# Performance work log

Measured on AMD Instinct MI355X. Metric: run time of the kernel, lower is better.

The kernel has to match this reference:

```python
import jax, jax.numpy as jnp
import numpy as np

# Perfect 8-ary tree, 6 levels, level-order node indexing.
K = 8            # children per internal node
D = 512          # embedding_dim
P = 8            # number of dependency types (num_params)
OFF = [0, 1, 9, 73, 585, 4681, 37449]  # level start offsets; N = 37449
N = OFF[-1]


def setup_inputs() -> dict:
    key = jax.random.key(0)
    ks = jax.random.split(key, 8)
    s = 1.0 / np.sqrt(D)  # torch default-ish init scale, avoids LSTM saturation
    return {
        "embeddings": jax.random.normal(ks[0], (N, D), dtype=jnp.float32),
        "dep_types": jax.random.randint(ks[1], (N,), 0, P, dtype=jnp.int32),
        "W_dep": jax.random.normal(ks[2], (P, D, D), dtype=jnp.float32) * s,
        "b_dep": jax.random.normal(ks[3], (P, D), dtype=jnp.float32) * s,
        "W_ih": jax.random.normal(ks[4], (4 * D, D), dtype=jnp.float32) * s,
        "W_hh": jax.random.normal(ks[5], (4 * D, D), dtype=jnp.float32) * s,
        "b_ih": jax.random.normal(ks[6], (4 * D,), dtype=jnp.float32) * s,
        "b_hh": jax.random.normal(ks[7], (4 * D,), dtype=jnp.float32) * s,
    }


def _lstm_final_c(seq, W_ih, W_hh, b_ih, b_hh):
    # seq: [B, T, D]; 1-layer LSTM with zero init state; returns final cell state c_T [B, D]
    B = seq.shape[0]
    h0 = jnp.zeros((B, D), seq.dtype)

    def step(carry, z_t):
        h, c = carry
        gates = z_t @ W_ih.T + h @ W_hh.T + b_ih + b_hh  # [B, 4D]
        i, f, g, o = jnp.split(gates, 4, axis=-1)        # torch gate order i,f,g,o
        i, f, o = jax.nn.sigmoid(i), jax.nn.sigmoid(f), jax.nn.sigmoid(o)
        g = jnp.tanh(g)
        c = f * c + i * g
        h = o * jnp.tanh(c)
        return (h, c), None

    (h, c), _ = jax.lax.scan(step, (h0, h0), jnp.swapaxes(seq, 0, 1))
    return c


def reference(embeddings, dep_types, W_dep, b_dep, W_ih, W_hh, b_ih, b_hh):
    # Leaves (level 5): LSTM over length-1 sequence [x] -> final cell state.
    leaf_x = embeddings[OFF[5]:OFF[6]]                       # [32768, D]
    z = _lstm_final_c(leaf_x[:, None, :], W_ih, W_hh, b_ih, b_hh)

    # Level-synchronous bottom-up sweep (exactly the recursion's per-node math).
    for l in range(4, -1, -1):
        m = OFF[l + 1] - OFF[l]                              # nodes at this level
        child_z = z.reshape(m, K, D)                         # children's subtree codes
        child_dep = dep_types[OFF[l + 1]:OFF[l + 2]].reshape(m, K)
        onehot = jax.nn.one_hot(child_dep, P, dtype=child_z.dtype)  # [m, K, P]
        # per-dep Linear: z_c = W_dep[dep] @ x_c + b_dep[dep]
        zc = jnp.einsum('mkj,pij,mkp->mki', child_z, W_dep, onehot) + onehot @ b_dep
        x = embeddings[OFF[l]:OFF[l + 1]]                    # node's own embedding, last in seq
        seq = jnp.concatenate([zc, x[:, None, :]], axis=1)   # [m, K+1, D]
        z = _lstm_final_c(seq, W_ih, W_hh, b_ih, b_hh)

    return z  # root sentence embedding, [1, D]
```

## Files before the change

kernel.cpp:

```cpp
#include <hip/hip_runtime.h>

typedef __attribute__((ext_vector_type(8))) short short8;
typedef __attribute__((ext_vector_type(4))) float f32x4;
typedef _Float16 half_t;

__device__ __forceinline__ unsigned short f2bf(float x){
  union { float f; unsigned u; } v; v.f = x;
  unsigned r = v.u + 0x7fffu + ((v.u >> 16) & 1u);
  return (unsigned short)(r >> 16);
}
__device__ __forceinline__ float sigm(float x){ return 1.0f / (1.0f + __expf(-x)); }
__device__ __forceinline__ float tanh_(float x){
  float e = __expf(2.0f * x);
  return 1.0f - 2.0f / (e + 1.0f);
}
__device__ __forceinline__ short8 load_bf8_f32(const float* p){
  float4 a = *(const float4*)p;
  float4 b = *(const float4*)(p + 4);
  short8 r;
  r[0]=(short)f2bf(a.x); r[1]=(short)f2bf(a.y); r[2]=(short)f2bf(a.z); r[3]=(short)f2bf(a.w);
  r[4]=(short)f2bf(b.x); r[5]=(short)f2bf(b.y); r[6]=(short)f2bf(b.z); r[7]=(short)f2bf(b.w);
  return r;
}
__device__ __forceinline__ f32x4 mfma16(short8 a, short8 b, f32x4 c){
  return __builtin_amdgcn_mfma_f32_16x16x32_bf16(a, b, c, 0, 0, 0);
}
__device__ __forceinline__ void gload16(const void* g, void* lds){
  __builtin_amdgcn_global_load_lds((const __attribute__((address_space(1))) void*)g,
                                   (__attribute__((address_space(3))) void*)lds, 16, 0, 0);
}
__device__ __forceinline__ f32x4 shfl_xor4(f32x4 v, int m){
  f32x4 r;
  r[0]=__shfl_xor(v[0],m); r[1]=__shfl_xor(v[1],m);
  r[2]=__shfl_xor(v[2],m); r[3]=__shfl_xor(v[3],m);
  return r;
}
__device__ __forceinline__ float pick4(f32x4 v, int k){
  float a = (k&1)? v[1] : v[0];
  float b = (k&1)? v[3] : v[2];
  return (k&2)? b : a;
}
__device__ __forceinline__ f32x4 sel4(f32x4 a0, f32x4 a1, f32x4 a2, f32x4 a3, int k){
  f32x4 x = (k&1)? a1 : a0;
  f32x4 y = (k&1)? a3 : a2;
  return (k&2)? y : x;
}

#define KLOOP_BODY(ABASE, BBASE)                                                     \
  for (int kt = 0; kt < 8; ++kt){                                                    \
    _Pragma("unroll")                                                                \
    for (int q = 0; q < 4; ++q){                                                     \
      gload16(ABASE[q] + kt*64, &As[(q*32 + w*8)*64]);                               \
      gload16(BBASE[q] + kt*64, &Bs[(q*32 + w*8)*64]);                               \
    }                                                                                \
    __syncthreads();                                                                 \
    _Pragma("unroll")                                                                \
    for (int kk = 0; kk < 2; ++kk){                                                  \
      short8 av[4], bv[4];                                                           \
      _Pragma("unroll")                                                              \
      for (int i = 0; i < 4; ++i) av[i] = *(const short8*)&As[(wm*64 + i*16 + r15)*64 + kk*32 + g4*8]; \
      _Pragma("unroll")                                                              \
      for (int i = 0; i < 4; ++i) bv[i] = *(const short8*)&Bs[(wn*64 + i*16 + r15)*64 + kk*32 + g4*8]; \
      _Pragma("unroll")                                                              \
      for (int i = 0; i < 4; ++i)                                                    \
        _Pragma("unroll")                                                            \
        for (int j = 0; j < 4; ++j) acc[i][j] = mfma16(av[i], bv[j], acc[i][j]);     \
    }                                                                                \
    __syncthreads();                                                                 \
  }

__global__ __launch_bounds__(256) void prep_kernel(
    const float* __restrict__ emb, const int* __restrict__ dep,
    const float* __restrict__ W_dep, const float* __restrict__ b_dep,
    const float* __restrict__ W_ih, const float* __restrict__ W_hh,
    const float* __restrict__ b_ih, const float* __restrict__ b_hh,
    unsigned short* __restrict__ embb, unsigned short* __restrict__ Wih_il,
    unsigned short* __restrict__ Whh_il, unsigned short* __restrict__ Wleaf,
    unsigned short* __restrict__ WdT, float* __restrict__ bsum, float* __restrict__ bc,
    int* __restrict__ perm, int* __restrict__ tile_p, int* __restrict__ meta)
{
  const int bid = blockIdx.x, tid = threadIdx.x;
  if (bid < 1024){
    for (size_t i = (size_t)bid*256 + tid; i < 2396736ull; i += 1024ull*256)
      *(short8*)(embb + i*8) = load_bf8_f32(emb + i*8);
  } else if (bid < 1536){
    int idx = (bid-1024)*256 + tid; int r = idx >> 6, c8 = idx & 63;
    int sr = (r & 3)*512 + (r >> 2);
    *(short8*)(Wih_il + (size_t)r*512 + c8*8) = load_bf8_f32(W_ih + (size_t)sr*512 + c8*8);
  } else if (bid < 2048){
    int idx = (bid-1536)*256 + tid; int r = idx >> 6, c8 = idx & 63;
    int sr = (r & 3)*512 + (r >> 2);
    *(short8*)(Whh_il + (size_t)r*512 + c8*8) = load_bf8_f32(W_hh + (size_t)sr*512 + c8*8);
  } else if (bid < 2304){
    int idx = (bid-2048)*256 + tid; int r = idx >> 6, c8 = idx & 63;
    int sr = ((r & 1) ? 2 : 0)*512 + (r >> 1);
    *(short8*)(Wleaf + (size_t)r*512 + c8*8) = load_bf8_f32(W_ih + (size_t)sr*512 + c8*8);
  } else if (bid < 2816){
    __shared__ unsigned short tle[64][65];
    int lb = bid - 2304; int p = lb >> 6; int tile = lb & 63;
    int i0 = (tile >> 3)*64, j0 = (tile & 7)*64;
    const float* src = W_dep + (size_t)p*512*512;
    for (int q = 0; q < 16; ++q){
      int e = q*256 + tid; int li = e >> 6, lj = e & 63;
      tle[li][lj] = f2bf(src[(size_t)(i0+li)*512 + (j0+lj)]);
    }
    __syncthreads();
    unsigned short* dst = WdT + (size_t)p*512*512;
    for (int q = 0; q < 16; ++q){
      int e = q*256 + tid; int lj = e >> 6, li = e & 63;
      dst[(size_t)(j0+lj)*512 + (i0+li)] = tle[li][lj];
    }
  } else if (bid < 2824){
    int r = (bid-2816)*256 + tid;
    if (r < 2048){ int g = r & 3, j = r >> 2; bsum[r] = b_ih[g*512+j] + b_hh[g*512+j]; }
  } else if (bid < 2888){
    __shared__ float bd[512];
    int lb = bid - 2824; int p = lb >> 3, ch = lb & 7;
    for (int i = tid; i < 512; i += 256) bd[i] = b_dep[p*512 + i];
    __syncthreads();
    int r = ch*256 + tid; int g = r & 3, j = r >> 2;
    const float* wr = W_ih + (size_t)(g*512 + j)*512;
    float s = 0.0f;
    for (int i = 0; i < 512; ++i) s = fmaf(wr[i], bd[i], s);
    bc[(size_t)p*2048 + r] = s;
  } else {
    __shared__ int cnt[8], base[8], fill[8];
    int lb = bid - 2888; const int l = lb >> 3, t = lb & 7;
    const int M_[5]  = {1,8,64,512,4096};
    const int CB_[5] = {1,9,73,585,4681};
    const int MT_[5] = {8,8,8,12,40};
    const int PB_[5] = {69632,61440,53248,40960,0};
    const int TB_[5] = {544,480,416,320,0};
    const int m = M_[l], cb = CB_[l], MT = MT_[l];
    int* pm = perm + PB_[l] + t*MT*128;
    int* tp = tile_p + TB_[l] + t*MT;
    if (tid < 8){ cnt[tid] = 0; fill[tid] = 0; }
    __syncthreads();
    for (int n = tid; n < m; n += 256) atomicAdd(&cnt[dep[cb + n*8 + t]], 1);
    __syncthreads();
    if (tid == 0){
      int tiles = 0;
      for (int p = 0; p < 8; ++p){
        base[p] = tiles*128;
        int g = (cnt[p] + 127) >> 7;
        for (int q = 0; q < g; ++q) tp[tiles + q] = p;
        tiles += g;
      }
      meta[l*8 + t] = tiles;
    }
    __syncthreads();
    for (int i = tid; i < MT*128; i += 256) pm[i] = -1;
    __syncthreads();
    for (int n = tid; n < m; n += 256){
      int p = dep[cb + n*8 + t];
      pm[base[p] + atomicAdd(&fill[p], 1)] = n;
    }
  }
}

__global__ __launch_bounds__(256) void combo_gemm(
    const unsigned short* __restrict__ A,
    const unsigned short* __restrict__ WdT,
    unsigned short* __restrict__ C)
{
  const int p  = blockIdx.x >> 6;
  const int mt = (blockIdx.x >> 2) & 15;
  const int nb = blockIdx.x & 3;
  __shared__ unsigned short As[128*64];
  __shared__ unsigned short Bs[128*64];
  const int tid = threadIdx.x, lane = tid & 63, w = tid >> 6;
  const int wm = w >> 1, wn = w & 1;
  const int r15 = lane & 15, g4 = lane >> 4;
  const int kc = (lane & 7)*8;

  const unsigned short* ab[4]; const unsigned short* bb[4];
  #pragma unroll
  for (int q = 0; q < 4; ++q){
    int rl = mt*128 + q*32 + w*8 + (lane >> 3);
    ab[q] = A + (size_t)rl*512 + kc;
    int br = nb*128 + q*32 + w*8 + (lane >> 3);
    bb[q] = WdT + (size_t)p*262144 + (size_t)br*512 + kc;
  }
  f32x4 acc[4][4] = {};
  KLOOP_BODY(ab, bb)
  unsigned short* Cp = C + (size_t)p*1048576;
  #pragma unroll
  for (int mi = 0; mi < 4; ++mi)
    #pragma unroll
    for (int ni = 0; ni < 4; ++ni)
      #pragma unroll
      for (int j = 0; j < 4; ++j){
        int row = mt*128 + wm*64 + mi*16 + g4*4 + j;
        int col = nb*128 + wn*64 + ni*16 + r15;
        Cp[(size_t)row*512 + col] = f2bf(acc[mi][ni][j]);
      }
}

__global__ __launch_bounds__(256) void leaf_gemm(
    const unsigned short* __restrict__ embL,
    const unsigned short* __restrict__ Wleaf,
    const float* __restrict__ bsum,
    unsigned short* __restrict__ zo)
{
  const int nb = blockIdx.x & 7;
  const int mt = blockIdx.x >> 3;
  __shared__ unsigned short As[128*64];
  __shared__ unsigned short Bs[128*64];
  const int tid = threadIdx.x, lane = tid & 63, w = tid >> 6;
  const int wm = w >> 1, wn = w & 1;
  const int r15 = lane & 15, g4 = lane >> 4;
  const int kc = (lane & 7)*8;

  const unsigned short* ab[4]; const unsigned short* bb[4];
  #pragma unroll
  for (int q = 0; q < 4; ++q){
    int rl = mt*128 + q*32 + w*8 + (lane >> 3);
    ab[q] = embL + (size_t)rl*512 + kc;
    int br = nb*128 + q*32 + w*8 + (lane >> 3);
    bb[q] = Wleaf + (size_t)br*512 + kc;
  }
  f32x4 acc[4][4] = {};
  KLOOP_BODY(ab, bb)
  const int g2 = r15 & 1;
  #pragma unroll
  for (int ni = 0; ni < 4; ++ni){
    int ci = nb*128 + wn*64 + ni*16 + r15;
    float b = bsum[4*(ci >> 1) + (g2 ? 2 : 0)];
    #pragma unroll
    for (int mi = 0; mi < 4; ++mi){
      acc[mi][ni][0]+=b; acc[mi][ni][1]+=b; acc[mi][ni][2]+=b; acc[mi][ni][3]+=b;
    }
  }
  #pragma unroll
  for (int mi = 0; mi < 4; ++mi)
    #pragma unroll
    for (int ni = 0; ni < 4; ++ni){
      f32x4 a0 = acc[mi][ni];
      f32x4 a1 = shfl_xor4(a0, 1);
      f32x4 vi_ = g2 ? a1 : a0;
      f32x4 vg_ = g2 ? a0 : a1;
      int jz = (nb*128 + wn*64 + ni*16 + r15) >> 1;
      #pragma unroll
      for (int u = 0; u < 2; ++u){
        int jrow = (g2 << 1) + u;
        float zi = pick4(vi_, jrow), zg = pick4(vg_, jrow);
        int row = mt*128 + wm*64 + mi*16 + g4*4 + jrow;
        zo[(size_t)row*512 + jz] = f2bf(sigm(zi) * tanh_(zg));
      }
    }
}

__device__ __forceinline__ void step_core(
    unsigned short* As, unsigned short* Bs,
    const unsigned short* __restrict__ embb,
    const unsigned short* __restrict__ Wcombo,
    const unsigned short* __restrict__ Wih_il,
    const unsigned short* __restrict__ Whh_il,
    const float* __restrict__ bsum, const float* __restrict__ bc,
    const unsigned short* __restrict__ zin, unsigned short* __restrict__ zo,
    const unsigned short* __restrict__ hi, unsigned short* __restrict__ ho,
    float* __restrict__ cbuf, float* __restrict__ outp,
    const int* __restrict__ pm, const int* __restrict__ tp,
    int node_base, int m, int t, int mt, int nbq, int l)
{
  const int tid = threadIdx.x, lane = tid & 63, w = tid >> 6;
  const int wm = w >> 1, wn = w & 1;
  const int r15 = lane & 15, g4 = lane >> 4;
  const int kc = (lane & 7)*8;
  const int first = (t == 0), last = (t == 8);
  const int p = tp ? tp[mt] : 0;

  int nn[4];
  #pragma unroll
  for (int q = 0; q < 4; ++q){
    int rl = mt*128 + q*32 + w*8 + (lane >> 3);
    int n = pm ? pm[rl] : (rl < m ? rl : -1);
    nn[q] = (n < 0) ? 0 : n;
  }
  f32x4 acc[4][4] = {};
  {
    const unsigned short* Bx = (t < 8) ? (Wcombo + (size_t)p*1048576) : Wih_il;
    const unsigned short* ab[4]; const unsigned short* bb[4];
    #pragma unroll
    for (int q = 0; q < 4; ++q){
      ab[q] = (t < 8) ? (zin + ((size_t)nn[q]*8 + t)*512 + kc)
                      : (embb + (size_t)(node_base + nn[q])*512 + kc);
      int br = nbq*128 + q*32 + w*8 + (lane >> 3);
      bb[q] = Bx + (size_t)br*512 + kc;
    }
    KLOOP_BODY(ab, bb)
  }
  if (!first){
    const unsigned short* ab[4]; const unsigned short* bb[4];
    #pragma unroll
    for (int q = 0; q < 4; ++q){
      ab[q] = hi + (size_t)nn[q]*512 + kc;
      int br = nbq*128 + q*32 + w*8 + (lane >> 3);
      bb[q] = Whh_il + (size_t)br*512 + kc;
    }
    KLOOP_BODY(ab, bb)
  }
  const int gate = r15 & 3;
  #pragma unroll
  for (int ni = 0; ni < 4; ++ni){
    int ci = nbq*128 + wn*64 + ni*16 + r15;
    float b = bsum[ci] + ((t < 8) ? bc[(size_t)p*2048 + ci] : 0.0f);
    #pragma unroll
    for (int mi = 0; mi < 4; ++mi){
      acc[mi][ni][0]+=b; acc[mi][ni][1]+=b; acc[mi][ni][2]+=b; acc[mi][ni][3]+=b;
    }
  }
  const int jr = r15 & 3;
  #pragma unroll
  for (int mi = 0; mi < 4; ++mi){
    int rl = mt*128 + wm*64 + mi*16 + g4*4 + jr;
    int n = pm ? pm[rl] : (rl < m ? rl : -1);
    #pragma unroll
    for (int ni = 0; ni < 4; ++ni){
      f32x4 a0 = acc[mi][ni];
      f32x4 a1 = shfl_xor4(a0, 1);
      f32x4 a2 = shfl_xor4(a0, 2);
      f32x4 a3 = shfl_xor4(a1, 2);
      f32x4 vi_ = sel4(a0,a1,a2,a3, gate);
      f32x4 vf_ = sel4(a0,a1,a2,a3, gate^1);
      f32x4 vg_ = sel4(a0,a1,a2,a3, gate^2);
      f32x4 vo_ = sel4(a0,a1,a2,a3, gate^3);
      float xi = pick4(vi_, jr), xf = pick4(vf_, jr);
      float xg = pick4(vg_, jr), xo = pick4(vo_, jr);
      if (n >= 0){
        int jz = nbq*32 + wn*16 + ni*4 + (r15 >> 2);
        size_t idx = (size_t)n*512 + jz;
        float i_ = sigm(xi), f_ = sigm(xf), g_ = tanh_(xg), o_ = sigm(xo);
        float cold = first ? 0.0f : cbuf[idx];
        float cn = fmaf(f_, cold, i_*g_);
        if (!last){ cbuf[idx] = cn; ho[idx] = f2bf(o_*tanh_(cn)); }
        else { if (l > 0) zo[idx] = f2bf(cn); else outp[idx] = cn; }
      }
    }
  }
}

__global__ __launch_bounds__(256) void step_kernel(
    const unsigned short* __restrict__ embb,
    const unsigned short* __restrict__ Wcombo,
    const unsigned short* __restrict__ Wih_il,
    const unsigned short* __restrict__ Whh_il,
    const float* __restrict__ bsum, const float* __restrict__ bc,
    const unsigned short* __restrict__ zin, unsigned short* __restrict__ zo,
    const unsigned short* __restrict__ hi, unsigned short* __restrict__ ho,
    float* __restrict__ cbuf, float* __restrict__ outp,
    const int* __restrict__ perm_t, const int* __restrict__ tile_t,
    const int* __restrict__ meta_t,
    int fixed_nt, int MTcap, int node_base, int m, int t, int l)
{
  __shared__ unsigned short As[128*64];
  __shared__ unsigned short Bs[128*64];
  int ntiles = meta_t ? *meta_t : fixed_nt;
  if (ntiles > MTcap) ntiles = MTcap;
  const int njobs = ntiles * 16;
  const int chunk = (njobs + 7) >> 3;
  const int g = blockIdx.x & 7, i = blockIdx.x >> 3;
  const int job = g*chunk + i;
  if (i >= chunk || job >= njobs) return;
  const int mt = job % ntiles, nbq = job / ntiles;
  step_core(As, Bs, embb, Wcombo, Wih_il, Whh_il, bsum, bc, zin, zo, hi, ho,
            cbuf, outp, perm_t, tile_t, node_base, m, t, mt, nbq, l);
}

__global__ __launch_bounds__(256) void gatex_kernel(
    const unsigned short* __restrict__ embb,
    const unsigned short* __restrict__ Wcombo,
    const unsigned short* __restrict__ Wih_il,
    const float* __restrict__ bsum, const float* __restrict__ bc,
    const unsigned short* __restrict__ zin,
    half_t* __restrict__ gx, unsigned short* __restrict__ h0out,
    float* __restrict__ cbuf,
    const int* __restrict__ perm_l, const int* __restrict__ tile_l,
    const int* __restrict__ meta_l,
    int MT, int m, int node_base)
{
  __shared__ unsigned short As[128*64];
  __shared__ unsigned short Bs[128*64];
  const int jt = blockIdx.x >> 4, nbq = blockIdx.x & 15;
  int t, mt, p = 0;
  const int* pm = nullptr;
  if (jt < 8*MT){
    t = jt / MT; mt = jt - t*MT;
    if (mt >= meta_l[t]) return;
    pm = perm_l + t*MT*128;
    p = tile_l[t*MT + mt];
  } else {
    t = 8; mt = jt - 8*MT;
  }
  const int tid = threadIdx.x, lane = tid & 63, w = tid >> 6;
  const int wm = w >> 1, wn = w & 1;
  const int r15 = lane & 15, g4 = lane >> 4;
  const int kc = (lane & 7)*8;

  int nn[4];
  #pragma unroll
  for (int q = 0; q < 4; ++q){
    int rl = mt*128 + q*32 + w*8 + (lane >> 3);
    int n = pm ? pm[rl] : (rl < m ? rl : -1);
    nn[q] = (n < 0) ? 0 : n;
  }
  const unsigned short* Bx = (t < 8) ? (Wcombo + (size_t)p*1048576) : Wih_il;
  const unsigned short* ab[4]; const unsigned short* bb[4];
  #pragma unroll
  for (int q = 0; q < 4; ++q){
    ab[q] = (t < 8) ? (zin + ((size_t)nn[q]*8 + t)*512 + kc)
                    : (embb + (size_t)(node_base + nn[q])*512 + kc);
    int br = nbq*128 + q*32 + w*8 + (lane >> 3);
    bb[q] = Bx + (size_t)br*512 + kc;
  }
  f32x4 acc[4][4] = {};
  KLOOP_BODY(ab, bb)

  #pragma unroll
  for (int ni = 0; ni < 4; ++ni){
    int ci = nbq*128 + wn*64 + ni*16 + r15;
    float b = bsum[ci] + ((t < 8) ? bc[(size_t)p*2048 + ci] : 0.0f);
    #pragma unroll
    for (int mi = 0; mi < 4; ++mi){
      acc[mi][ni][0]+=b; acc[mi][ni][1]+=b; acc[mi][ni][2]+=b; acc[mi][ni][3]+=b;
    }
  }

  if (t == 0){
    const int gate = r15 & 3;
    const int jr = r15 & 3;
    #pragma unroll
    for (int mi = 0; mi < 4; ++mi){
      int rl = mt*128 + wm*64 + mi*16 + g4*4 + jr;
      int n = pm ? pm[rl] : (rl < m ? rl : -1);
      #pragma unroll
      for (int ni = 0; ni < 4; ++ni){
        f32x4 a0 = acc[mi][ni];
        f32x4 a1 = shfl_xor4(a0, 1);
        f32x4 a2 = shfl_xor4(a0, 2);
        f32x4 a3 = shfl_xor4(a1, 2);
        f32x4 vi_ = sel4(a0,a1,a2,a3, gate);
        f32x4 vg_ = sel4(a0,a1,a2,a3, gate^2);
        f32x4 vo_ = sel4(a0,a1,a2,a3, gate^3);
        float xi = pick4(vi_, jr);
        float xg = pick4(vg_, jr);
        float xo = pick4(vo_, jr);
        if (n >= 0){
          int jz = nbq*32 + wn*16 + ni*4 + (r15 >> 2);
          size_t idx = (size_t)n*512 + jz;
          float cn = sigm(xi) * tanh_(xg);
          cbuf[idx] = cn;
          h0out[idx] = f2bf(sigm(xo) * tanh_(cn));
        }
      }
    }
  } else {
    #pragma unroll
    for (int mi = 0; mi < 4; ++mi)
      #pragma unroll
      for (int ni = 0; ni < 4; ++ni){
        int ci = nbq*128 + wn*64 + ni*16 + r15;
        #pragma unroll
        for (int j = 0; j < 4; ++j){
          int rl = mt*128 + wm*64 + mi*16 + g4*4 + j;
          int n = pm ? pm[rl] : (rl < m ? rl : -1);
          if (n >= 0) gx[((size_t)t*m + n)*2048 + ci] = (half_t)acc[mi][ni][j];
        }
      }
  }
}

__global__ __launch_bounds__(256) void hstep_kernel(
    const unsigned short* __restrict__ Whh_il,
    const half_t* __restrict__ gx,
    const unsigned short* __restrict__ hi, unsigned short* __restrict__ ho,
    float* __restrict__ cbuf,
    unsigned short* __restrict__ zo, float* __restrict__ outp,
    int m, int t, int last)
{
  __shared__ unsigned short As[128*64];
  __shared__ unsigned short Bs[128*64];
  const int mt = blockIdx.x >> 4, nbq = blockIdx.x & 15;
  const int tid = threadIdx.x, lane = tid & 63, w = tid >> 6;
  const int wm = w >> 1, wn = w & 1;
  const int r15 = lane & 15, g4 = lane >> 4;
  const int kc = (lane & 7)*8;

  int nn[4];
  #pragma unroll
  for (int q = 0; q < 4; ++q){
    int rl = mt*128 + q*32 + w*8 + (lane >> 3);
    nn[q] = (rl < m) ? rl : 0;
  }
  const unsigned short* ab[4]; const unsigned short* bb[4];
  #pragma unroll
  for (int q = 0; q < 4; ++q){
    ab[q] = hi + (size_t)nn[q]*512 + kc;
    int br = nbq*128 + q*32 + w*8 + (lane >> 3);
    bb[q] = Whh_il + (size_t)br*512 + kc;
  }
  f32x4 acc[4][4] = {};
  KLOOP_BODY(ab, bb)

  #pragma unroll
  for (int mi = 0; mi < 4; ++mi)
    #pragma unroll
    for (int ni = 0; ni < 4; ++ni){
      int ci = nbq*128 + wn*64 + ni*16 + r15;
      #pragma unroll
      for (int j = 0; j < 4; ++j){
        int rl = mt*128 + wm*64 + mi*16 + g4*4 + j;
        if (rl < m) acc[mi][ni][j] += (float)gx[((size_t)t*m + rl)*2048 + ci];
      }
    }

  const int gate = r15 & 3;
  const int jr = r15 & 3;
  #pragma unroll
  for (int mi = 0; mi < 4; ++mi){
    int rl = mt*128 + wm*64 + mi*16 + g4*4 + jr;
    int n = (rl < m) ? rl : -1;
    #pragma unroll
    for (int ni = 0; ni < 4; ++ni){
      f32x4 a0 = acc[mi][ni];
      f32x4 a1 = shfl_xor4(a0, 1);
      f32x4 a2 = shfl_xor4(a0, 2);
      f32x4 a3 = shfl_xor4(a1, 2);
      f32x4 vi_ = sel4(a0,a1,a2,a3, gate);
      f32x4 vf_ = sel4(a0,a1,a2,a3, gate^1);
      f32x4 vg_ = sel4(a0,a1,a2,a3, gate^2);
      f32x4 vo_ = sel4(a0,a1,a2,a3, gate^3);
      float xi = pick4(vi_, jr), xf = pick4(vf_, jr);
      float xg = pick4(vg_, jr), xo = pick4(vo_, jr);
      if (n >= 0){
        int jz = nbq*32 + wn*16 + ni*4 + (r15 >> 2);
        size_t idx = (size_t)n*512 + jz;
        float i_ = sigm(xi), f_ = sigm(xf), g_ = tanh_(xg), o_ = sigm(xo);
        float cn = fmaf(f_, cbuf[idx], i_*g_);
        if (!last){ cbuf[idx] = cn; ho[idx] = f2bf(o_*tanh_(cn)); }
        else { if (zo) zo[idx] = f2bf(cn); else outp[idx] = cn; }
      }
    }
  }
}

extern "C" void kernel_launch(void* const* d_in, const int* in_sizes, int n_in,
                              void* d_out, int out_size, void* d_ws, size_t ws_size,
                              hipStream_t stream)
{
  (void)in_sizes; (void)n_in; (void)out_size; (void)ws_size;
  const float* emb   = (const float*)d_in[0];
  const int*   dep   = (const int*)  d_in[1];
  const float* W_dep = (const float*)d_in[2];
  const float* b_dep = (const float*)d_in[3];
  const float* W_ih  = (const float*)d_in[4];
  const float* W_hh  = (const float*)d_in[5];
  const float* b_ih  = (const float*)d_in[6];
  const float* b_hh  = (const float*)d_in[7];
  float* out = (float*)d_out;

  unsigned short* embb   = (unsigned short*)d_ws;
  unsigned short* Wih_il = embb   + 19173888ull;
  unsigned short* Whh_il = Wih_il + 1048576ull;
  unsigned short* Wleaf  = Whh_il + 1048576ull;
  unsigned short* WdT    = Wleaf  + 524288ull;
  unsigned short* Wcombo = WdT    + 2097152ull;
  unsigned short* Z0     = Wcombo + 8388608ull;
  unsigned short* Z1     = Z0     + 16777216ull;
  unsigned short* hA     = Z1     + 2097152ull;
  unsigned short* hB     = hA     + 2097152ull;
  float* cbuf  = (float*)(hB + 2097152ull);
  float* bsum  = cbuf + 2097152ull;
  float* bc    = bsum + 2048;
  int*  perm   = (int*)(bc + 16384);
  int*  tile_p = perm + 77824;
  int*  meta   = tile_p + 608;
  half_t* gx   = (half_t*)(meta + 40);

  prep_kernel<<<2928, 256, 0, stream>>>(emb, dep, W_dep, b_dep, W_ih, W_hh, b_ih, b_hh,
                                        embb, Wih_il, Whh_il, Wleaf, WdT, bsum, bc,
                                        perm, tile_p, meta);
  combo_gemm<<<512, 256, 0, stream>>>(Wih_il, WdT, Wcombo);
  leaf_gemm<<<2048, 256, 0, stream>>>(embb + (size_t)4681*512, Wleaf, bsum, Z0);

  for (int t = 0; t <= 8; ++t){
    const unsigned short* hi = (t & 1) ? hA : hB;
    unsigned short* ho       = (t & 1) ? hB : hA;
    int grid = (t < 8) ? 40*16 : 32*16;
    step_kernel<<<grid, 256, 0, stream>>>(
        embb, Wcombo, Wih_il, Whh_il, bsum, bc,
        Z0, Z1, hi, ho, cbuf, nullptr,
        (t < 8) ? (perm + t*40*128) : nullptr,
        (t < 8) ? (tile_p + t*40) : nullptr,
        (t < 8) ? (meta + 4*8 + t) : nullptr,
        32, 40, 585, 4096, t, 4);
  }

  struct LvP { int m, MT, PB, TB, nb_, mtiles; };
  const LvP LP[4] = {
    {512, 12, 40960, 320, 73, 4},
    {64,  8,  53248, 416, 9,  1},
    {8,   8,  61440, 480, 1,  1},
    {1,   8,  69632, 544, 0,  1}};
  for (int k = 0; k < 4; ++k){
    const int l = 3 - k;
    const unsigned short* zin = (l & 1) ? Z1 : Z0;
    unsigned short* zo        = (l & 1) ? Z0 : Z1;
    gatex_kernel<<<(8*LP[k].MT + LP[k].mtiles)*16, 256, 0, stream>>>(
        embb, Wcombo, Wih_il, bsum, bc, zin, gx, hA, cbuf,
        perm + LP[k].PB, tile_p + LP[k].TB, meta + l*8,
        LP[k].MT, LP[k].m, LP[k].nb_);
    for (int t = 1; t <= 8; ++t){
      const unsigned short* hi = (t & 1) ? hA : hB;
      unsigned short* ho       = (t & 1) ? hB : hA;
      hstep_kernel<<<LP[k].mtiles*16, 256, 0, stream>>>(
          Whh_il, gx, hi, ho, cbuf,
          (l > 0) ? zo : nullptr, (l == 0) ? out : nullptr,
          LP[k].m, t, (t == 8));
    }
  }
}
```

Baseline: 1.539 ms.

## Double-buffer LDS tiles and XOR-swizzle layout in shared GEMM k-loop

The shared k-loop macro now keeps two LDS buffers per operand and issues the global-to-LDS loads for the next k-tile before computing on the current one. This overlaps memory latency with MFMA work and drops one barrier per iteration. The global load column offset is also XOR-swizzled by row, with matching swizzled LDS reads, to cut bank conflicts. LDS per block doubles to 64 KB, which may lower occupancy.

```diff
diff --git a/kernel.cpp b/kernel.cpp
--- a/kernel.cpp
+++ b/kernel.cpp
@@ -47,26 +47,41 @@
 }
 
 #define KLOOP_BODY(ABASE, BBASE)                                                     \
-  for (int kt = 0; kt < 8; ++kt){                                                    \
+  {                                                                                  \
     _Pragma("unroll")                                                                \
     for (int q = 0; q < 4; ++q){                                                     \
-      gload16(ABASE[q] + kt*64, &As[(q*32 + w*8)*64]);                               \
-      gload16(BBASE[q] + kt*64, &Bs[(q*32 + w*8)*64]);                               \
+      gload16(ABASE[q], As + (q*32 + w*8)*64);                                       \
+      gload16(BBASE[q], Bs + (q*32 + w*8)*64);                                       \
     }                                                                                \
     __syncthreads();                                                                 \
-    _Pragma("unroll")                                                                \
-    for (int kk = 0; kk < 2; ++kk){                                                  \
-      short8 av[4], bv[4];                                                           \
+    for (int kt = 0; kt < 8; ++kt){                                                  \
+      unsigned short* Ac = As + (kt & 1)*8192;                                       \
+      unsigned short* Bc = Bs + (kt & 1)*8192;                                       \
+      if (kt < 7){                                                                   \
+        unsigned short* An = As + ((kt + 1) & 1)*8192;                               \
+        unsigned short* Bn = Bs + ((kt + 1) & 1)*8192;                               \
+        _Pragma("unroll")                                                            \
+        for (int q = 0; q < 4; ++q){                                                 \
+          gload16(ABASE[q] + (kt+1)*64, An + (q*32 + w*8)*64);                       \
+          gload16(BBASE[q] + (kt+1)*64, Bn + (q*32 + w*8)*64);                       \
+        }                                                                            \
+      }                                                                              \
       _Pragma("unroll")                                                              \
-      for (int i = 0; i < 4; ++i) av[i] = *(const short8*)&As[(wm*64 + i*16 + r15)*64 + kk*32 + g4*8]; \
-      _Pragma("unroll")                                                              \
-      for (int i = 0; i < 4; ++i) bv[i] = *(const short8*)&Bs[(wn*64 + i*16 + r15)*64 + kk*32 + g4*8]; \
-      _Pragma("unroll")                                                              \
-      for (int i = 0; i < 4; ++i)                                                    \
+      for (int kk = 0; kk < 2; ++kk){                                                \
+        short8 av[4], bv[4];                                                         \
         _Pragma("unroll")                                                            \
-        for (int j = 0; j < 4; ++j) acc[i][j] = mfma16(av[i], bv[j], acc[i][j]);     \
+        for (int i = 0; i < 4; ++i)                                                  \
+          av[i] = *(const short8*)&Ac[(wm*64 + i*16 + r15)*64 + (((kk*4 + g4) ^ (r15 & 7))*8)]; \
+        _Pragma("unroll")                                                            \
+        for (int i = 0; i < 4; ++i)                                                  \
+          bv[i] = *(const short8*)&Bc[(wn*64 + i*16 + r15)*64 + (((kk*4 + g4) ^ (r15 & 7))*8)]; \
+        _Pragma("unroll")                                                            \
+        for (int i = 0; i < 4; ++i)                                                  \
+          _Pragma("unroll")                                                          \
+          for (int j = 0; j < 4; ++j) acc[i][j] = mfma16(av[i], bv[j], acc[i][j]);   \
+      }                                                                              \
+      __syncthreads();                                                               \
     }                                                                                \
-    __syncthreads();                                                                 \
   }
 
 __global__ __launch_bounds__(256) void prep_kernel(
@@ -166,12 +181,12 @@
   const int p  = blockIdx.x >> 6;
   const int mt = (blockIdx.x >> 2) & 15;
   const int nb = blockIdx.x & 3;
-  __shared__ unsigned short As[128*64];
-  __shared__ unsigned short Bs[128*64];
+  __shared__ unsigned short As[16384];
+  __shared__ unsigned short Bs[16384];
   const int tid = threadIdx.x, lane = tid & 63, w = tid >> 6;
   const int wm = w >> 1, wn = w & 1;
   const int r15 = lane & 15, g4 = lane >> 4;
-  const int kc = (lane & 7)*8;
+  const int kc = ((lane & 7) ^ (lane >> 3)) * 8;
 
   const unsigned short* ab[4]; const unsigned short* bb[4];
   #pragma unroll
@@ -204,12 +219,12 @@
 {
   const int nb = blockIdx.x & 7;
   const int mt = blockIdx.x >> 3;
-  __shared__ unsigned short As[128*64];
-  __shared__ unsigned short Bs[128*64];
+  __shared__ unsigned short As[16384];
+  __shared__ unsigned short Bs[16384];
   const int tid = threadIdx.x, lane = tid & 63, w = tid >> 6;
   const int wm = w >> 1, wn = w & 1;
   const int r15 = lane & 15, g4 = lane >> 4;
-  const int kc = (lane & 7)*8;
+  const int kc = ((lane & 7) ^ (lane >> 3)) * 8;
 
   const unsigned short* ab[4]; const unsigned short* bb[4];
   #pragma unroll
@@ -266,7 +281,7 @@
   const int tid = threadIdx.x, lane = tid & 63, w = tid >> 6;
   const int wm = w >> 1, wn = w & 1;
   const int r15 = lane & 15, g4 = lane >> 4;
-  const int kc = (lane & 7)*8;
+  const int kc = ((lane & 7) ^ (lane >> 3)) * 8;
   const int first = (t == 0), last = (t == 8);
   const int p = tp ? tp[mt] : 0;
 
@@ -353,8 +368,8 @@
     const int* __restrict__ meta_t,
     int fixed_nt, int MTcap, int node_base, int m, int t, int l)
 {
-  __shared__ unsigned short As[128*64];
-  __shared__ unsigned short Bs[128*64];
+  __shared__ unsigned short As[16384];
+  __shared__ unsigned short Bs[16384];
   int ntiles = meta_t ? *meta_t : fixed_nt;
   if (ntiles > MTcap) ntiles = MTcap;
   const int njobs = ntiles * 16;
@@ -379,8 +394,8 @@
     const int* __restrict__ meta_l,
     int MT, int m, int node_base)
 {
-  __shared__ unsigned short As[128*64];
-  __shared__ unsigned short Bs[128*64];
+  __shared__ unsigned short As[16384];
+  __shared__ unsigned short Bs[16384];
   const int jt = blockIdx.x >> 4, nbq = blockIdx.x & 15;
   int t, mt, p = 0;
   const int* pm = nullptr;
@@ -395,7 +410,7 @@
   const int tid = threadIdx.x, lane = tid & 63, w = tid >> 6;
   const int wm = w >> 1, wn = w & 1;
   const int r15 = lane & 15, g4 = lane >> 4;
-  const int kc = (lane & 7)*8;
+  const int kc = ((lane & 7) ^ (lane >> 3)) * 8;
 
   int nn[4];
   #pragma unroll
@@ -478,13 +493,13 @@
     unsigned short* __restrict__ zo, float* __restrict__ outp,
     int m, int t, int last)
 {
-  __shared__ unsigned short As[128*64];
-  __shared__ unsigned short Bs[128*64];
+  __shared__ unsigned short As[16384];
+  __shared__ unsigned short Bs[16384];
   const int mt = blockIdx.x >> 4, nbq = blockIdx.x & 15;
   const int tid = threadIdx.x, lane = tid & 63, w = tid >> 6;
   const int wm = w >> 1, wn = w & 1;
   const int r15 = lane & 15, g4 = lane >> 4;
-  const int kc = (lane & 7)*8;
+  const int kc = ((lane & 7) ^ (lane >> 3)) * 8;
 
   int nn[4];
   #pragma unroll
```

After: 1.381 ms. 10.2% less time.

## XOR-swizzle LDS tile layout in all GEMM kernels and reorder leaf_gemm blocks

Applied to the files above, without the earlier changes.

Applies an XOR swizzle to the 16-byte chunk column in the shared-memory A/B tiles, both on the global-to-LDS load side (kc) and on the MFMA fragment read side. This targets LDS bank conflicts in the fragment reads, where rows at a 128-byte stride map onto the same banks. It also remaps leaf_gemm's block index so that consecutive blocks share an N-tile of Wleaf across spread-out M-tiles, which changes cache reuse. The loop is split into stage and compute macros, but the synchronisation structure stays the same.

```diff
diff --git a/kernel.cpp b/kernel.cpp
--- a/kernel.cpp
+++ b/kernel.cpp
@@ -46,26 +46,38 @@
   return (k&2)? y : x;
 }
 
-#define KLOOP_BODY(ABASE, BBASE)                                                     \
-  for (int kt = 0; kt < 8; ++kt){                                                    \
+#define KSTAGE1(AB, BB, off)                                                         \
+  {                                                                                  \
     _Pragma("unroll")                                                                \
     for (int q = 0; q < 4; ++q){                                                     \
-      gload16(ABASE[q] + kt*64, &As[(q*32 + w*8)*64]);                               \
-      gload16(BBASE[q] + kt*64, &Bs[(q*32 + w*8)*64]);                               \
+      gload16(AB[q] + (off), As + (q*32 + w*8)*64);                                  \
+      gload16(BB[q] + (off), Bs + (q*32 + w*8)*64);                                  \
     }                                                                                \
-    __syncthreads();                                                                 \
+  }
+
+#define KCOMP1                                                                       \
+  {                                                                                  \
     _Pragma("unroll")                                                                \
     for (int kk = 0; kk < 2; ++kk){                                                  \
       short8 av[4], bv[4];                                                           \
       _Pragma("unroll")                                                              \
-      for (int i = 0; i < 4; ++i) av[i] = *(const short8*)&As[(wm*64 + i*16 + r15)*64 + kk*32 + g4*8]; \
+      for (int i = 0; i < 4; ++i)                                                    \
+        av[i] = *(const short8*)&As[(wm*64 + i*16 + r15)*64 + (((kk*4 + g4) ^ (r15 & 7))*8)]; \
       _Pragma("unroll")                                                              \
-      for (int i = 0; i < 4; ++i) bv[i] = *(const short8*)&Bs[(wn*64 + i*16 + r15)*64 + kk*32 + g4*8]; \
+      for (int i = 0; i < 4; ++i)                                                    \
+        bv[i] = *(const short8*)&Bs[(wn*64 + i*16 + r15)*64 + (((kk*4 + g4) ^ (r15 & 7))*8)]; \
       _Pragma("unroll")                                                              \
       for (int i = 0; i < 4; ++i)                                                    \
         _Pragma("unroll")                                                            \
         for (int j = 0; j < 4; ++j) acc[i][j] = mfma16(av[i], bv[j], acc[i][j]);     \
     }                                                                                \
+  }
+
+#define KLOOP1(AB, BB)                                                               \
+  for (int kt = 0; kt < 8; ++kt){                                                    \
+    KSTAGE1(AB, BB, kt*64)                                                           \
+    __syncthreads();                                                                 \
+    KCOMP1                                                                           \
     __syncthreads();                                                                 \
   }
 
@@ -166,12 +178,12 @@
   const int p  = blockIdx.x >> 6;
   const int mt = (blockIdx.x >> 2) & 15;
   const int nb = blockIdx.x & 3;
-  __shared__ unsigned short As[128*64];
-  __shared__ unsigned short Bs[128*64];
+  __shared__ unsigned short As[8192];
+  __shared__ unsigned short Bs[8192];
   const int tid = threadIdx.x, lane = tid & 63, w = tid >> 6;
   const int wm = w >> 1, wn = w & 1;
   const int r15 = lane & 15, g4 = lane >> 4;
-  const int kc = (lane & 7)*8;
+  const int kc = ((lane & 7) ^ (lane >> 3)) * 8;
 
   const unsigned short* ab[4]; const unsigned short* bb[4];
   #pragma unroll
@@ -182,7 +194,7 @@
     bb[q] = WdT + (size_t)p*262144 + (size_t)br*512 + kc;
   }
   f32x4 acc[4][4] = {};
-  KLOOP_BODY(ab, bb)
+  KLOOP1(ab, bb)
   unsigned short* Cp = C + (size_t)p*1048576;
   #pragma unroll
   for (int mi = 0; mi < 4; ++mi)
@@ -202,14 +214,14 @@
     const float* __restrict__ bsum,
     unsigned short* __restrict__ zo)
 {
-  const int nb = blockIdx.x & 7;
-  const int mt = blockIdx.x >> 3;
-  __shared__ unsigned short As[128*64];
-  __shared__ unsigned short Bs[128*64];
+  const int mt = (blockIdx.x & 7)*32 + ((blockIdx.x >> 3) & 31);
+  const int nb = blockIdx.x >> 8;
+  __shared__ unsigned short As[8192];
+  __shared__ unsigned short Bs[8192];
   const int tid = threadIdx.x, lane = tid & 63, w = tid >> 6;
   const int wm = w >> 1, wn = w & 1;
   const int r15 = lane & 15, g4 = lane >> 4;
-  const int kc = (lane & 7)*8;
+  const int kc = ((lane & 7) ^ (lane >> 3)) * 8;
 
   const unsigned short* ab[4]; const unsigned short* bb[4];
   #pragma unroll
@@ -220,7 +232,7 @@
     bb[q] = Wleaf + (size_t)br*512 + kc;
   }
   f32x4 acc[4][4] = {};
-  KLOOP_BODY(ab, bb)
+  KLOOP1(ab, bb)
   const int g2 = r15 & 1;
   #pragma unroll
   for (int ni = 0; ni < 4; ++ni){
@@ -266,7 +278,7 @@
   const int tid = threadIdx.x, lane = tid & 63, w = tid >> 6;
   const int wm = w >> 1, wn = w & 1;
   const int r15 = lane & 15, g4 = lane >> 4;
-  const int kc = (lane & 7)*8;
+  const int kc = ((lane & 7) ^ (lane >> 3)) * 8;
   const int first = (t == 0), last = (t == 8);
   const int p = tp ? tp[mt] : 0;
 
@@ -288,7 +300,7 @@
       int br = nbq*128 + q*32 + w*8 + (lane >> 3);
       bb[q] = Bx + (size_t)br*512 + kc;
     }
-    KLOOP_BODY(ab, bb)
+    KLOOP1(ab, bb)
   }
   if (!first){
     const unsigned short* ab[4]; const unsigned short* bb[4];
@@ -298,7 +310,7 @@
       int br = nbq*128 + q*32 + w*8 + (lane >> 3);
       bb[q] = Whh_il + (size_t)br*512 + kc;
     }
-    KLOOP_BODY(ab, bb)
+    KLOOP1(ab, bb)
   }
   const int gate = r15 & 3;
   #pragma unroll
@@ -353,8 +365,8 @@
     const int* __restrict__ meta_t,
     int fixed_nt, int MTcap, int node_base, int m, int t, int l)
 {
-  __shared__ unsigned short As[128*64];
-  __shared__ unsigned short Bs[128*64];
+  __shared__ unsigned short As[8192];
+  __shared__ unsigned short Bs[8192];
   int ntiles = meta_t ? *meta_t : fixed_nt;
   if (ntiles > MTcap) ntiles = MTcap;
   const int njobs = ntiles * 16;
@@ -379,8 +391,8 @@
     const int* __restrict__ meta_l,
     int MT, int m, int node_base)
 {
-  __shared__ unsigned short As[128*64];
-  __shared__ unsigned short Bs[128*64];
+  __shared__ unsigned short As[8192];
+  __shared__ unsigned short Bs[8192];
   const int jt = blockIdx.x >> 4, nbq = blockIdx.x & 15;
   int t, mt, p = 0;
   const int* pm = nullptr;
@@ -395,7 +407,7 @@
   const int tid = threadIdx.x, lane = tid & 63, w = tid >> 6;
   const int wm = w >> 1, wn = w & 1;
   const int r15 = lane & 15, g4 = lane >> 4;
-  const int kc = (lane & 7)*8;
+  const int kc = ((lane & 7) ^ (lane >> 3)) * 8;
 
   int nn[4];
   #pragma unroll
@@ -414,7 +426,7 @@
     bb[q] = Bx + (size_t)br*512 + kc;
   }
   f32x4 acc[4][4] = {};
-  KLOOP_BODY(ab, bb)
+  KLOOP1(ab, bb)
 
   #pragma unroll
   for (int ni = 0; ni < 4; ++ni){
@@ -478,13 +490,13 @@
     unsigned short* __restrict__ zo, float* __restrict__ outp,
     int m, int t, int last)
 {
-  __shared__ unsigned short As[128*64];
-  __shared__ unsigned short Bs[128*64];
+  __shared__ unsigned short As[8192];
+  __shared__ unsigned short Bs[8192];
   const int mt = blockIdx.x >> 4, nbq = blockIdx.x & 15;
   const int tid = threadIdx.x, lane = tid & 63, w = tid >> 6;
   const int wm = w >> 1, wn = w & 1;
   const int r15 = lane & 15, g4 = lane >> 4;
-  const int kc = (lane & 7)*8;
+  const int kc = ((lane & 7) ^ (lane >> 3)) * 8;
 
   int nn[4];
   #pragma unroll
@@ -500,7 +512,7 @@
     bb[q] = Whh_il + (size_t)br*512 + kc;
   }
   f32x4 acc[4][4] = {};
-  KLOOP_BODY(ab, bb)
+  KLOOP1(ab, bb)
 
   #pragma unroll
   for (int mi = 0; mi < 4; ++mi)
```

Measured after the change: 1.407 ms. 8.6% less time.
